# Kernel optimization log

Hardware: AMD Instinct MI355X
Metric: run time of the kernel (lower is better)

Reference implementation:

```python
import jax, jax.numpy as jnp
import numpy as np

PRE_NMS_THRESH = 0.05
PRE_NMS_TOP_N = 200
NMS_THRESH = 0.5
FPN_POST_NMS_TOP_N = 100
MIN_SIZE = 0.0
NUM_CLASSES = 2
C = NUM_CLASSES - 1
NB = 2
STRIDES = (8, 16, 32, 64, 128)
HS = (100, 50, 25, 13, 7)
WS = (128, 64, 32, 16, 8)
IMG_H, IMG_W = 800, 1024
MAXV = 8  # max #vertices of quad-clipped-by-quad polygon


def _shoelace_fixed(V, n):
    # area of polygon stored in fixed buffer V[MAXV,2] with n valid vertices
    a = jnp.asarray(0.0, V.dtype)
    for k in range(MAXV):
        nxt = jnp.where(jnp.equal(k, n - 1), 0, k + 1)
        term = V[k, 0] * V[nxt, 1] - V[nxt, 0] * V[k, 1]
        a = a + jnp.where(k < n, term, 0.0)
    return 0.5 * jnp.abs(a)


def _quad_area(Q):  # Q: [4,2]
    x, y = Q[:, 0], Q[:, 1]
    return 0.5 * jnp.abs(jnp.sum(x * jnp.roll(y, -1) - jnp.roll(x, -1) * y))


def _clip_halfplane(V, n, p1, p2, orient):
    # Sutherland-Hodgman clip of polygon (V,n) against directed edge p1->p2
    d = p2 - p1

    def side(p):
        return orient * (d[0] * (p[1] - p1[1]) - d[1] * (p[0] - p1[0]))

    out = jnp.zeros((MAXV, 2), V.dtype)
    cnt = jnp.int32(0)
    for k in range(MAXV):
        cur = V[k]
        prev = V[jnp.where(jnp.equal(k, 0), n - 1, k - 1)]
        sc = side(cur)
        sp = side(prev)
        cur_in = sc >= 0.0
        prev_in = sp >= 0.0
        denom = sp - sc
        t = sp / jnp.where(jnp.abs(denom) > 1e-9, denom, 1e-9)
        ip = prev + t * (cur - prev)
        valid = k < n
        emit_ip = valid & (cur_in != prev_in)
        out = jnp.where(emit_ip, out.at[cnt].set(ip, mode='drop'), out)
        cnt = cnt + emit_ip.astype(jnp.int32)
        emit_cur = valid & cur_in
        out = jnp.where(emit_cur, out.at[cnt].set(cur, mode='drop'), out)
        cnt = cnt + emit_cur.astype(jnp.int32)
    return out, cnt


def _poly_inter_area(A, B):  # A,B: [4,2] convex quads
    sB = jnp.sum(B[:, 0] * jnp.roll(B[:, 1], -1) - jnp.roll(B[:, 0], -1) * B[:, 1])
    orient = jnp.where(sB >= 0.0, 1.0, -1.0)
    V = jnp.zeros((MAXV, 2), A.dtype).at[:4].set(A)
    n = jnp.int32(4)
    for e in range(4):
        V, n = _clip_halfplane(V, n, B[e], B[(e + 1) % 4], orient)
    return _shoelace_fixed(V, n)


def _process_level(loc, cls_l, reg_l, image_sizes):
    Nb, Cc, H, W = cls_l.shape
    # (N,C,H,W) -> (N,HW*C) with index = (h*W+w)*C + c (matches permute/reshape)
    scores = jax.nn.sigmoid(cls_l.transpose(0, 2, 3, 1).reshape(Nb, H * W * Cc))
    cand = scores > PRE_NMS_THRESH
    masked = jnp.where(cand, scores, 0.0)
    k = min(PRE_NMS_TOP_N, H * W * Cc)
    vals, idx = jax.lax.top_k(masked, k)
    loc_idx = idx // Cc
    labels = idx % Cc + 1
    regr = reg_l.transpose(0, 2, 3, 1).reshape(Nb, H * W, 8)
    reg_g = jnp.take_along_axis(regr, loc_idx[..., None], axis=1)  # [Nb,k,8]
    loc_g = loc[loc_idx]  # [Nb,k,2]
    poly = jnp.tile(loc_g, (1, 1, 4)) - reg_g  # (x-r0, y-r1, ..., x-r6, y-r7)
    hh = image_sizes[:, 0].astype(poly.dtype)[:, None, None]
    ww = image_sizes[:, 1].astype(poly.dtype)[:, None, None]
    xs = jnp.clip(poly[..., 0::2], 0.0, ww - 1.0)
    ys = jnp.clip(poly[..., 1::2], 0.0, hh - 1.0)
    poly = jnp.stack([xs, ys], axis=-1).reshape(Nb, k, 8)
    valid = vals > PRE_NMS_THRESH
    bw = xs.max(-1) - xs.min(-1)
    bh = ys.max(-1) - ys.min(-1)
    valid = valid & (bw >= MIN_SIZE) & (bh >= MIN_SIZE)
    sc = jnp.where(valid, jnp.sqrt(vals), 0.0)
    return poly, sc, labels, valid


def _nms_single(poly, scores, labels, valid):
    T = scores.shape[0]
    order = jnp.argsort(-scores)
    poly = poly[order]
    scores = scores[order]
    labels = labels[order]
    valid = valid[order]
    quads = poly.reshape(T, 4, 2)

    def pairwise_iou(q):
        inter = jax.vmap(jax.vmap(_poly_inter_area, (None, 0)), (0, None))(q, q)
        areas = jax.vmap(_quad_area)(q)
        union = areas[:, None] + areas[None, :] - inter
        return inter / jnp.maximum(union, 1e-9)

    # IoU only feeds boolean suppression decisions -> no gradient flows through it
    iou = jax.lax.stop_gradient(pairwise_iou(quads))
    ar = jnp.arange(T)

    def body(i, keep):
        sup = (iou[i] > NMS_THRESH) & (ar > i)
        return jnp.where(keep[i], keep & ~sup, keep)

    keep = jax.lax.stop_gradient(jax.lax.fori_loop(0, T, body, valid))
    final = jnp.where(keep, scores, -1.0)
    top_s, top_i = jax.lax.top_k(final, FPN_POST_NMS_TOP_N)
    ok = top_s > 0.0
    return poly[top_i], jnp.where(ok, top_s, 0.0), labels[top_i], ok


def _forward(locs, clss, regs, image_sizes):
    parts = [_process_level(l, c, r, image_sizes) for l, c, r in zip(locs, clss, regs)]
    poly = jnp.concatenate([p[0] for p in parts], axis=1)
    sc = jnp.concatenate([p[1] for p in parts], axis=1)
    lab = jnp.concatenate([p[2] for p in parts], axis=1)
    val = jnp.concatenate([p[3] for p in parts], axis=1)
    return jax.vmap(_nms_single)(poly, sc, lab, val)


def setup_inputs() -> dict:
    key = jax.random.key(0)
    inp = {}
    k = key
    for i, (h, w, s) in enumerate(zip(HS, WS, STRIDES)):
        k, k1, k2, k3 = jax.random.split(k, 4)
        sx = jnp.arange(w, dtype=jnp.float32) * s + s // 2
        sy = jnp.arange(h, dtype=jnp.float32) * s + s // 2
        yy, xx = jnp.meshgrid(sy, sx, indexing='ij')
        inp[f'locations_l{i}'] = jnp.stack([xx.reshape(-1), yy.reshape(-1)], axis=1)
        inp[f'box_cls_l{i}'] = jax.random.normal(k1, (NB, C, h, w), dtype=jnp.float32)
        inp[f'box_reg_l{i}'] = jax.random.normal(k2, (NB, 8, h, w), dtype=jnp.float32) * (2.0 * s)
        inp[f'centerness_l{i}'] = jax.random.normal(k3, (NB, 1, h, w), dtype=jnp.float32)
    inp['image_sizes'] = jnp.array([[IMG_H, IMG_W]] * NB, dtype=jnp.int32)
    return inp


def reference(locations_l0, locations_l1, locations_l2, locations_l3, locations_l4,
              box_cls_l0, box_cls_l1, box_cls_l2, box_cls_l3, box_cls_l4,
              box_reg_l0, box_reg_l1, box_reg_l2, box_reg_l3, box_reg_l4,
              centerness_l0, centerness_l1, centerness_l2, centerness_l3, centerness_l4,
              image_sizes):
    # centerness is accepted but unused, matching the original module's forward
    locs = [locations_l0, locations_l1, locations_l2, locations_l3, locations_l4]
    clss = [box_cls_l0, box_cls_l1, box_cls_l2, box_cls_l3, box_cls_l4]
    regs = [box_reg_l0, box_reg_l1, box_reg_l2, box_reg_l3, box_reg_l4]
    boxes, scores, labels, valid = _forward(locs, clss, regs, image_sizes)
    return boxes, scores, labels, valid
```

## Files before the change

### kernel.cpp

```cpp
#include <hip/hip_runtime.h>

#pragma clang fp contract(off)

#define T_CAND 856
#define NW 14
#define NSH 16
#define HSTR 513

__device__ const int d_HW[5]  = {12800, 3200, 800, 208, 56};
__device__ const int d_K[5]   = {200, 200, 200, 200, 56};
__device__ const int d_OFF[5] = {0, 200, 400, 600, 800};

struct LevelPtrs {
  const float* loc[5];
  const float* cls[5];
  const float* reg[5];
  const int*   img;
};

__device__ __forceinline__ unsigned long long readlane64(unsigned long long v, int lane) {
  const unsigned lo = (unsigned)__builtin_amdgcn_readlane((int)(unsigned)(v & 0xFFFFFFFFULL), lane);
  const unsigned hi = (unsigned)__builtin_amdgcn_readlane((int)(unsigned)(v >> 32), lane);
  return ((unsigned long long)hi << 32) | lo;
}
__device__ __forceinline__ unsigned long long rfl64(unsigned long long v) {
  const unsigned lo = (unsigned)__builtin_amdgcn_readfirstlane((int)(unsigned)(v & 0xFFFFFFFFULL));
  const unsigned hi = (unsigned)__builtin_amdgcn_readfirstlane((int)(unsigned)(v >> 32));
  return ((unsigned long long)hi << 32) | lo;
}

__global__ __launch_bounds__(1024) void topk_kernel(LevelPtrs P,
    float* __restrict__ candPoly, float* __restrict__ candSc, unsigned* __restrict__ candValid,
    unsigned* __restrict__ pairCount) {
  __shared__ unsigned hist[NSH * HSTR];
  __shared__ unsigned histT[512];
  __shared__ __align__(16) unsigned long long gbuf[1024];
  __shared__ float mcache[12800];
  __shared__ int gcount;
  __shared__ int cutB;
  const int blk = blockIdx.x;
  const int b = blk / 5, l = blk % 5;
  const int HW = d_HW[l], K = d_K[l], OFF = d_OFF[l];
  const float* cls = P.cls[l] + (size_t)b * HW;
  const float* reg = P.reg[l] + (size_t)b * 8 * HW;
  const float* loc = P.loc[l];
  const int tid = threadIdx.x;
  const int wave = tid >> 6, lane = tid & 63;

  if (blk == 0 && tid == 0) *pairCount = 0u;
  for (int t = tid; t < NSH * HSTR; t += 1024) hist[t] = 0u;
  if (tid == 0) gcount = 0;
  __syncthreads();

  const int sh = (tid >> 2) & (NSH - 1);
  for (int idx = tid; idx < HW; idx += 1024) {
    const float x = cls[idx];
    const float s = (float)(1.0 / (1.0 + exp(-(double)x)));
    const float m = (s > 0.05f) ? s : 0.0f;
    mcache[idx] = m;
    atomicAdd(&hist[sh * HSTR + (__float_as_uint(m) >> 21)], 1u);
  }
  __syncthreads();
  for (int t = tid; t < 512; t += 1024) {
    unsigned sum = 0;
#pragma unroll
    for (int h = 0; h < NSH; ++h) sum += hist[h * HSTR + t];
    histT[t] = sum;
  }
  __syncthreads();
  if (wave == 0) {
    const int t0 = lane * 8;
    int h[8], loc8[8];
#pragma unroll
    for (int k = 0; k < 8; ++k) h[k] = (int)histT[t0 + k];
    int run = 0;
#pragma unroll
    for (int k = 7; k >= 0; --k) { run += h[k]; loc8[k] = run; }
    int v = run;
#pragma unroll
    for (int d = 1; d < 64; d <<= 1) {
      const int u = __shfl_down(v, d);
      if (lane + d < 64) v += u;
    }
    const int excl = v - run;
    int cand = -1;
#pragma unroll
    for (int k = 7; k >= 0; --k)
      if (cand < 0 && excl + loc8[k] >= K) cand = t0 + k;
    const unsigned long long bal = __ballot(cand >= 0);
    const int hi = 63 - __builtin_clzll(bal);
    const int cb = __shfl(cand, hi);
    if (lane == 0) cutB = cb;
  }
  __syncthreads();

  const int cb = cutB;
  for (int idx = tid; idx < HW; idx += 1024) {
    const unsigned kb = __float_as_uint(mcache[idx]);
    if ((int)(kb >> 21) >= cb) {
      const int pos = atomicAdd(&gcount, 1);
      if (pos < 1024)
        gbuf[pos] = ((unsigned long long)kb << 32)
                  | (unsigned long long)(0xFFFFFFFFu - (unsigned)idx);
    }
  }
  __syncthreads();
  const int G = min(gcount, 1024);
  if (tid < 4 && G + tid < 1024) gbuf[G + tid] = 0ULL;
  __syncthreads();

  if (tid < G) {
    const unsigned long long my = gbuf[tid];
    const int G4 = (G + 3) & ~3;
    int rank = 0;
    const ulonglong2* g2 = (const ulonglong2*)gbuf;
    for (int j = 0; j < G4 / 2; j += 2) {
      const ulonglong2 a = g2[j], c = g2[j + 1];
      rank += (a.x > my) ? 1 : 0;
      rank += (a.y > my) ? 1 : 0;
      rank += (c.x > my) ? 1 : 0;
      rank += (c.y > my) ? 1 : 0;
    }
    if (rank < K) {
      const float val = __uint_as_float((unsigned)(my >> 32));
      const int idx = (int)(0xFFFFFFFFu - (unsigned)(my & 0xFFFFFFFFULL));
      const float hh = (float)P.img[b * 2 + 0];
      const float ww = (float)P.img[b * 2 + 1];
      const float xmax = ww - 1.0f, ymax = hh - 1.0f;
      const float lx = loc[idx * 2 + 0], ly = loc[idx * 2 + 1];
      const int go = b * T_CAND + OFF + rank;
#pragma unroll
      for (int q = 0; q < 4; ++q) {
        const float rx = reg[(2 * q + 0) * HW + idx];
        const float ry = reg[(2 * q + 1) * HW + idx];
        const float pxv = fminf(fmaxf(lx - rx, 0.0f), xmax);
        const float pyv = fminf(fmaxf(ly - ry, 0.0f), ymax);
        candPoly[go * 8 + 2 * q + 0] = pxv;
        candPoly[go * 8 + 2 * q + 1] = pyv;
      }
      const bool v = (val > 0.05f);
      candSc[go]    = v ? sqrtf(val) : 0.0f;
      candValid[go] = v ? 1u : 0u;
    }
  }
}

__global__ __launch_bounds__(1024) void sort_kernel(
    const float* __restrict__ candPoly, const float* __restrict__ candSc,
    const unsigned* __restrict__ candValid,
    float* __restrict__ sPoly, float* __restrict__ sSc, unsigned* __restrict__ sValid,
    float* __restrict__ sAABB) {
  __shared__ __align__(16) unsigned long long key[T_CAND];
  const int b = blockIdx.x, tid = threadIdx.x;
  float sc = 0.0f;
  if (tid < T_CAND) {
    sc = candSc[b * T_CAND + tid];
    key[tid] = ((unsigned long long)__float_as_uint(sc) << 32)
             | (unsigned long long)(0xFFFFFFFFu - (unsigned)tid);
  }
  __syncthreads();
  if (tid < T_CAND) {
    const unsigned long long my = key[tid];
    int rank = 0;
    const ulonglong2* k2 = (const ulonglong2*)key;
    for (int j = 0; j < T_CAND / 2; j += 2) {
      const ulonglong2 a = k2[j], c = k2[j + 1];
      rank += (a.x > my) ? 1 : 0;
      rank += (a.y > my) ? 1 : 0;
      rank += (c.x > my) ? 1 : 0;
      rank += (c.y > my) ? 1 : 0;
    }
    sSc[b * T_CAND + rank]    = sc;
    sValid[b * T_CAND + rank] = candValid[b * T_CAND + tid];
    const float4* src = (const float4*)(candPoly + (size_t)(b * T_CAND + tid) * 8);
    const float4 s0 = src[0], s1 = src[1];
    float4* dst = (float4*)(sPoly + (size_t)(b * T_CAND + rank) * 8);
    dst[0] = s0;
    dst[1] = s1;
    float4 bb;
    bb.x = fminf(fminf(s0.x, s0.z), fminf(s1.x, s1.z));
    bb.y = fminf(fminf(s0.y, s0.w), fminf(s1.y, s1.w));
    bb.z = fmaxf(fmaxf(s0.x, s0.z), fmaxf(s1.x, s1.z));
    bb.w = fmaxf(fmaxf(s0.y, s0.w), fmaxf(s1.y, s1.w));
    *(float4*)(sAABB + (size_t)(b * T_CAND + rank) * 4) = bb;
  }
}

__global__ __launch_bounds__(256) void pairs_kernel(
    const unsigned* __restrict__ sValid, const float* __restrict__ sAABB,
    unsigned long long* __restrict__ MT, unsigned* __restrict__ pairList,
    unsigned* __restrict__ pairCount) {
  __shared__ __align__(16) float4 ra[64];
  __shared__ unsigned rv[64];
  __shared__ unsigned long long cw[64];
  __shared__ int rowoff[64];
  __shared__ int lcnt;
  __shared__ int gbase;
  const int b = blockIdx.y;
  int it = 0, rem = blockIdx.x;
  while (rem >= NW - it) { rem -= NW - it; ++it; }
  const int jt = it + rem;
  const int tid = threadIdx.x;
  const int wave = tid >> 6, lane = tid & 63;

  if (tid == 0) lcnt = 0;
  if (tid < 64) {
    const int row = it * 64 + tid;
    const int rc = row < T_CAND ? row : (T_CAND - 1);
    ra[tid] = *(const float4*)(sAABB + (size_t)(b * T_CAND + rc) * 4);
    rv[tid] = (row < T_CAND) ? sValid[b * T_CAND + row] : 0u;
    if (row < T_CAND) MT[((size_t)b * NW + jt) * T_CAND + row] = 0ULL;
  }
  __syncthreads();

  const int j = jt * 64 + lane;
  const int jcl = j < T_CAND ? j : (T_CAND - 1);
  const float4 jb = *(const float4*)(sAABB + (size_t)(b * T_CAND + jcl) * 4);
  const bool jv = (j < T_CAND) && (sValid[b * T_CAND + jcl] != 0u);
#pragma unroll
  for (int k = 0; k < 16; ++k) {
    const int r = wave * 16 + k;
    const int irow = it * 64 + r;
    const float4 ib = ra[r];
    const bool iv = rv[r] != 0u;
    const bool ov = !(ib.z < jb.x || jb.z < ib.x || ib.w < jb.y || jb.w < ib.y);
    const bool pred = iv && jv && (j > irow) && ov;
    const unsigned long long w = __ballot(pred);
    if (lane == 0) cw[r] = w;
  }
  __syncthreads();
  if (tid < 64) {
    const int c = __popcll(cw[tid]);
    rowoff[tid] = c ? atomicAdd(&lcnt, c) : 0;
  }
  __syncthreads();
  if (tid == 0) gbase = lcnt ? (int)atomicAdd(pairCount, (unsigned)lcnt) : 0;
  __syncthreads();
  if (tid < 64) {
    unsigned long long w = cw[tid];
    unsigned off = (unsigned)(gbase + rowoff[tid]);
    const int iRow = it * 64 + tid;
    while (w) {
      const int jo = (int)__builtin_ctzll(w);
      w &= w - 1;
      pairList[off++] = ((unsigned)b << 20) | ((unsigned)iRow << 10) | (unsigned)(jt * 64 + jo);
    }
  }
}

__global__ __launch_bounds__(256) void clip_kernel(
    const unsigned* __restrict__ pairList, const unsigned* __restrict__ pairCount,
    const float* __restrict__ sPoly, unsigned long long* __restrict__ MT) {
  const int tid = threadIdx.x;
  const unsigned count = *pairCount;
  for (unsigned t0 = blockIdx.x * 256 + tid; t0 < count; t0 += gridDim.x * 256) {
    const unsigned pk = pairList[t0];
    const int b = (pk >> 20) & 1, i = (pk >> 10) & 1023, j = pk & 1023;
    const float4* Ap4 = (const float4*)(sPoly + (size_t)(b * T_CAND + i) * 8);
    const float4 a01 = Ap4[0], a23 = Ap4[1];
    const float ax0 = a01.x, ay0 = a01.y, ax1 = a01.z, ay1 = a01.w,
                ax2 = a23.x, ay2 = a23.y, ax3 = a23.z, ay3 = a23.w;
    const float4* Bp4 = (const float4*)(sPoly + (size_t)(b * T_CAND + j) * 8);
    const float4 b01 = Bp4[0], b23 = Bp4[1];
    const float bx0 = b01.x, by0 = b01.y, bx1 = b01.z, by1 = b01.w,
                bx2 = b23.x, by2 = b23.y, bx3 = b23.z, by3 = b23.w;
    float sB = bx0 * by1 - bx1 * by0;
    sB += bx1 * by2 - bx2 * by1;
    sB += bx2 * by3 - bx3 * by2;
    sB += bx3 * by0 - bx0 * by3;
    const float orient = (sB >= 0.0f) ? 1.0f : -1.0f;
    float aA = ax0 * ay1 - ax1 * ay0;
    aA += ax1 * ay2 - ax2 * ay1;
    aA += ax2 * ay3 - ax3 * ay2;
    aA += ax3 * ay0 - ax0 * ay3;

    float s0x = ax0, s0y = ay0, s1x = ax1, s1y = ay1,
          s2x = ax2, s2y = ay2, s3x = ax3, s3y = ay3,
          s4x = 0.f, s4y = 0.f, s5x = 0.f, s5y = 0.f,
          s6x = 0.f, s6y = 0.f, s7x = 0.f, s7y = 0.f;
    int n = 4;
    float lastx = ax3, lasty = ay3;
    const float bex[5] = {bx0, bx1, bx2, bx3, bx0};
    const float bey[5] = {by0, by1, by2, by3, by0};

#define PUSH(w_, vx_, vy_)                                              \
    {                                                                   \
      const bool w__ = (w_);                                            \
      const float vx__ = (vx_), vy__ = (vy_);                           \
      t0x = (w__ && cnt == 0) ? vx__ : t0x; t0y = (w__ && cnt == 0) ? vy__ : t0y; \
      t1x = (w__ && cnt == 1) ? vx__ : t1x; t1y = (w__ && cnt == 1) ? vy__ : t1y; \
      t2x = (w__ && cnt == 2) ? vx__ : t2x; t2y = (w__ && cnt == 2) ? vy__ : t2y; \
      t3x = (w__ && cnt == 3) ? vx__ : t3x; t3y = (w__ && cnt == 3) ? vy__ : t3y; \
      t4x = (w__ && cnt == 4) ? vx__ : t4x; t4y = (w__ && cnt == 4) ? vy__ : t4y; \
      t5x = (w__ && cnt == 5) ? vx__ : t5x; t5y = (w__ && cnt == 5) ? vy__ : t5y; \
      t6x = (w__ && cnt == 6) ? vx__ : t6x; t6y = (w__ && cnt == 6) ? vy__ : t6y; \
      t7x = (w__ && cnt == 7) ? vx__ : t7x; t7y = (w__ && cnt == 7) ? vy__ : t7y; \
      nlx = (w__ && cnt < 8) ? vx__ : nlx;  nly = (w__ && cnt < 8) ? vy__ : nly;  \
      cnt += w__ ? 1 : 0;                                               \
    }

#define CLIP_K(k_, sx_, sy_)                                            \
    {                                                                   \
      const bool act = (k_) < n;                                        \
      const float cx = sx_, cy = sy_;                                   \
      const float sc2 = orient * (dx * (cy - p1y) - dy * (cx - p1x));   \
      const bool cin = (sc2 >= 0.0f), pin = (sp >= 0.0f);               \
      const float den = sp - sc2;                                       \
      const float dd = (fabsf(den) > 1e-9f) ? den : 1e-9f;              \
      const float tt = sp / dd;                                         \
      const float ipx = px + tt * (cx - px);                            \
      const float ipy = py + tt * (cy - py);                            \
      PUSH(act && (cin != pin), ipx, ipy);                              \
      PUSH(act && cin, cx, cy);                                         \
      px = cx; py = cy; sp = sc2;                                       \
    }

#pragma unroll
    for (int e = 0; e < 4; ++e) {
      const float p1x = bex[e], p1y = bey[e];
      const float dx = bex[e + 1] - p1x, dy = bey[e + 1] - p1y;
      float t0x = 0.f, t0y = 0.f, t1x = 0.f, t1y = 0.f, t2x = 0.f, t2y = 0.f,
            t3x = 0.f, t3y = 0.f, t4x = 0.f, t4y = 0.f, t5x = 0.f, t5y = 0.f,
            t6x = 0.f, t6y = 0.f, t7x = 0.f, t7y = 0.f;
      float nlx = lastx, nly = lasty;
      int cnt = 0;
      float px = lastx, py = lasty;
      float sp = orient * (dx * (py - p1y) - dy * (px - p1x));
      CLIP_K(0, s0x, s0y) CLIP_K(1, s1x, s1y) CLIP_K(2, s2x, s2y) CLIP_K(3, s3x, s3y)
      CLIP_K(4, s4x, s4y) CLIP_K(5, s5x, s5y) CLIP_K(6, s6x, s6y) CLIP_K(7, s7x, s7y)
      s0x = t0x; s0y = t0y; s1x = t1x; s1y = t1y; s2x = t2x; s2y = t2y;
      s3x = t3x; s3y = t3y; s4x = t4x; s4y = t4y; s5x = t5x; s5y = t5y;
      s6x = t6x; s6y = t6y; s7x = t7x; s7y = t7y;
      lastx = nlx; lasty = nly;
      n = cnt;
    }
#undef CLIP_K
#undef PUSH

    float a = 0.0f;
#define SHOE(k_, xk_, yk_, xn_, yn_)                                    \
    {                                                                   \
      const bool act = (k_) < n;                                        \
      const bool wrap = (k_) == n - 1;                                  \
      const float xn = wrap ? s0x : (xn_);                              \
      const float yn = wrap ? s0y : (yn_);                              \
      const float term = (xk_) * yn - xn * (yk_);                       \
      a += act ? term : 0.0f;                                           \
    }
    SHOE(0, s0x, s0y, s1x, s1y) SHOE(1, s1x, s1y, s2x, s2y)
    SHOE(2, s2x, s2y, s3x, s3y) SHOE(3, s3x, s3y, s4x, s4y)
    SHOE(4, s4x, s4y, s5x, s5y) SHOE(5, s5x, s5y, s6x, s6y)
    SHOE(6, s6x, s6y, s7x, s7y) SHOE(7, s7x, s7y, s7x, s7y)
#undef SHOE
    const float inter = 0.5f * fabsf(a);
    const float areaA = 0.5f * fabsf(aA);
    const float areaB = 0.5f * fabsf(sB);
    const float uni = areaA + areaB - inter;
    const float iou = inter / fmaxf(uni, 1e-9f);
    if (iou > 0.5f)
      atomicOr(&MT[((size_t)b * NW + (j >> 6)) * T_CAND + i], 1ULL << (j & 63));
  }
}

__global__ __launch_bounds__(1024) void nms_resolve_emit_kernel(
    const unsigned long long* __restrict__ MT, const unsigned* __restrict__ sValid,
    const float* __restrict__ sPoly, const float* __restrict__ sSc, float* __restrict__ out) {
  __shared__ __align__(16) unsigned long long mt[NW * T_CAND];
  __shared__ unsigned long long vb[16];
  __shared__ unsigned long long kw[NW];
  const int b = blockIdx.x;
  const int tid = threadIdx.x;
  const int wave = tid >> 6, lane = tid & 63;

  {
    const ulonglong2* g2 = (const ulonglong2*)(MT + (size_t)b * NW * T_CAND);
    ulonglong2* l2 = (ulonglong2*)mt;
    for (int t = tid; t < NW * T_CAND / 2; t += 1024) l2[t] = g2[t];
  }
  if (wave < NW) {
    const int idx = wave * 64 + lane;
    const bool v = (idx < T_CAND) && (sValid[b * T_CAND + idx] != 0u);
    const unsigned long long ball = __ballot(v);
    if (lane == 0) vb[wave] = ball;
  }
  __syncthreads();

  if (wave == 0) {
    unsigned long long kwreg = 0ULL;
    for (int q = 0; q < NW; ++q) {
      const unsigned long long* col = &mt[q * T_CAND];
      const int nrow = q * 64 + lane;
      const unsigned long long sup = col[nrow < T_CAND ? nrow : (T_CAND - 1)];
      unsigned long long acc = 0ULL;
      for (int wp = 0; wp < q; ++wp) {
        const unsigned long long row = col[wp * 64 + lane];
        const unsigned long long kword = readlane64(kwreg, wp);
        acc |= ((kword >> lane) & 1ULL) ? row : 0ULL;
      }
#pragma unroll
      for (int m = 1; m < 64; m <<= 1)
        acc |= (unsigned long long)__shfl_xor((long long)acc, m, 64);
      const unsigned long long S = rfl64(acc);
      const unsigned long long validq = rfl64(vb[q]);
      unsigned long long alive = validq & ~S;
      const unsigned long long suppr = __ballot(sup != 0ULL);
      unsigned long long rem = alive & suppr;
      while (rem) {
        const int s = (int)__builtin_ctzll(rem);
        rem &= rem - 1;
        if ((alive >> s) & 1ULL) {
          alive &= ~readlane64(sup, s);
          rem &= alive;
        }
      }
      if (lane == q) kwreg = alive;
    }
    if (lane < NW) kw[lane] = kwreg;
  }
  __syncthreads();

  if (tid < 100) {
    const int o = tid;
    int totalKeep = 0;
    for (int w = 0; w < NW; ++w) totalKeep += __popcll(kw[w]);
    const bool kept = o < totalKeep;
    int idx = 0;
    if (kept) {
      int r = o, w = 0;
      unsigned long long word = 0ULL;
      for (; w < NW; ++w) {
        word = kw[w];
        const int c = __popcll(word);
        if (r < c) break;
        r -= c;
      }
      for (int p = 0; p < r; ++p) word &= word - 1;
      idx = w * 64 + (__ffsll(word) - 1);
    } else {
      int r = o - totalKeep, w = 0;
      unsigned long long word = 0ULL;
      for (; w < NW; ++w) {
        const unsigned long long mk = (w == NW - 1) ? ((1ULL << (T_CAND - 64 * (NW - 1))) - 1ULL)
                                                    : ~0ULL;
        word = (~kw[w]) & mk;
        const int c = __popcll(word);
        if (r < c) break;
        r -= c;
      }
      for (int p = 0; p < r; ++p) word &= word - 1;
      idx = w * 64 + (__ffsll(word) - 1);
    }
    const float4* pp = (const float4*)(sPoly + (size_t)(b * T_CAND + idx) * 8);
    float4* ob2 = (float4*)(out + (size_t)b * 800 + (size_t)o * 8);
    ob2[0] = pp[0];
    ob2[1] = pp[1];
    out[1600 + b * 100 + o] = kept ? sSc[b * T_CAND + idx] : 0.0f;
    out[1800 + b * 100 + o] = 1.0f;
    out[2000 + b * 100 + o] = kept ? 1.0f : 0.0f;
  }
}

extern "C" void kernel_launch(void* const* d_in, const int* in_sizes, int n_in,
                              void* d_out, int out_size, void* d_ws, size_t ws_size,
                              hipStream_t stream) {
  (void)n_in; (void)out_size; (void)ws_size;
  LevelPtrs P;
  const bool interleaved = (in_sizes[2] == 204800);
  for (int l = 0; l < 5; ++l) {
    if (interleaved) {
      P.loc[l] = (const float*)d_in[4 * l + 0];
      P.cls[l] = (const float*)d_in[4 * l + 1];
      P.reg[l] = (const float*)d_in[4 * l + 2];
    } else {
      P.loc[l] = (const float*)d_in[l];
      P.cls[l] = (const float*)d_in[5 + l];
      P.reg[l] = (const float*)d_in[10 + l];
    }
  }
  P.img = (const int*)d_in[20];

  char* ws = (char*)d_ws;
  float*    candPoly  = (float*)(ws + 0);
  float*    candSc    = (float*)(ws + 54784);
  unsigned* candValid = (unsigned*)(ws + 61632);
  float*    sPoly     = (float*)(ws + 68480);
  float*    sSc       = (float*)(ws + 123264);
  unsigned* sValid    = (unsigned*)(ws + 130112);
  unsigned long long* MT = (unsigned long long*)(ws + 136960);
  float*    sAABB     = (float*)(ws + 328704);
  unsigned* pairCount = (unsigned*)(ws + 356096);
  unsigned* pairList  = (unsigned*)(ws + 356112);

  topk_kernel<<<dim3(10), dim3(1024), 0, stream>>>(P, candPoly, candSc, candValid, pairCount);
  sort_kernel<<<dim3(2), dim3(1024), 0, stream>>>(candPoly, candSc, candValid,
                                                  sPoly, sSc, sValid, sAABB);
  pairs_kernel<<<dim3((NW * (NW + 1)) / 2, 2), dim3(256), 0, stream>>>(sValid, sAABB, MT,
                                                                       pairList, pairCount);
  clip_kernel<<<dim3(512), dim3(256), 0, stream>>>(pairList, pairCount, sPoly, MT);
  nms_resolve_emit_kernel<<<dim3(2), dim3(1024), 0, stream>>>(MT, sValid, sPoly, sSc,
                                                              (float*)d_out);
}
```

Measured before the change: 74.75 us.

## Fuse five NMS stages into one cooperative kernel with grid syncs

Replaces the five separate kernel launches (top-k, sort, pair finding, polygon clipping, NMS resolve) with a single cooperative kernel of 210 blocks of 512 threads, separated by grid.sync(). The pair list is now built per tile in shared memory, and clipping results are OR-ed into shared words instead of going through a global pair list and atomic counter. The aim is to cut launch overhead and global round-trips between stages. In exchange it adds grid-wide barrier cost, leaves most blocks idle in the top-k and resolve phases, and uses a single large shared buffer that may limit occupancy.

```diff
diff --git a/kernel.cpp b/kernel.cpp
--- a/kernel.cpp
+++ b/kernel.cpp
@@ -1,4 +1,5 @@
 #include <hip/hip_runtime.h>
+#include <hip/hip_cooperative_groups.h>
 
 #pragma clang fp contract(off)
 
@@ -6,6 +7,10 @@
 #define NW 14
 #define NSH 16
 #define HSTR 513
+#define NBLK 210
+#define NTHR 512
+
+namespace cg = cooperative_groups;
 
 __device__ const int d_HW[5]  = {12800, 3200, 800, 208, 56};
 __device__ const int d_K[5]   = {200, 200, 200, 200, 56};
@@ -29,434 +34,423 @@
   return ((unsigned long long)hi << 32) | lo;
 }
 
-__global__ __launch_bounds__(1024) void topk_kernel(LevelPtrs P,
+__device__ __forceinline__ bool clip_hit(const float* __restrict__ sPoly, int b, int i, int j) {
+  const float4* Ap4 = (const float4*)(sPoly + (size_t)(b * T_CAND + i) * 8);
+  const float4 a01 = Ap4[0], a23 = Ap4[1];
+  const float ax0 = a01.x, ay0 = a01.y, ax1 = a01.z, ay1 = a01.w,
+              ax2 = a23.x, ay2 = a23.y, ax3 = a23.z, ay3 = a23.w;
+  const float4* Bp4 = (const float4*)(sPoly + (size_t)(b * T_CAND + j) * 8);
+  const float4 b01 = Bp4[0], b23 = Bp4[1];
+  const float bx0 = b01.x, by0 = b01.y, bx1 = b01.z, by1 = b01.w,
+              bx2 = b23.x, by2 = b23.y, bx3 = b23.z, by3 = b23.w;
+  float sB = bx0 * by1 - bx1 * by0;
+  sB += bx1 * by2 - bx2 * by1;
+  sB += bx2 * by3 - bx3 * by2;
+  sB += bx3 * by0 - bx0 * by3;
+  const float orient = (sB >= 0.0f) ? 1.0f : -1.0f;
+  float aA = ax0 * ay1 - ax1 * ay0;
+  aA += ax1 * ay2 - ax2 * ay1;
+  aA += ax2 * ay3 - ax3 * ay2;
+  aA += ax3 * ay0 - ax0 * ay3;
+
+  float s0x = ax0, s0y = ay0, s1x = ax1, s1y = ay1,
+        s2x = ax2, s2y = ay2, s3x = ax3, s3y = ay3,
+        s4x = 0.f, s4y = 0.f, s5x = 0.f, s5y = 0.f,
+        s6x = 0.f, s6y = 0.f, s7x = 0.f, s7y = 0.f;
+  int n = 4;
+  float lastx = ax3, lasty = ay3;
+  const float bex[5] = {bx0, bx1, bx2, bx3, bx0};
+  const float bey[5] = {by0, by1, by2, by3, by0};
+
+#define PUSH(w_, vx_, vy_)                                              \
+  {                                                                     \
+    const bool w__ = (w_);                                              \
+    const float vx__ = (vx_), vy__ = (vy_);                             \
+    t0x = (w__ && cnt == 0) ? vx__ : t0x; t0y = (w__ && cnt == 0) ? vy__ : t0y; \
+    t1x = (w__ && cnt == 1) ? vx__ : t1x; t1y = (w__ && cnt == 1) ? vy__ : t1y; \
+    t2x = (w__ && cnt == 2) ? vx__ : t2x; t2y = (w__ && cnt == 2) ? vy__ : t2y; \
+    t3x = (w__ && cnt == 3) ? vx__ : t3x; t3y = (w__ && cnt == 3) ? vy__ : t3y; \
+    t4x = (w__ && cnt == 4) ? vx__ : t4x; t4y = (w__ && cnt == 4) ? vy__ : t4y; \
+    t5x = (w__ && cnt == 5) ? vx__ : t5x; t5y = (w__ && cnt == 5) ? vy__ : t5y; \
+    t6x = (w__ && cnt == 6) ? vx__ : t6x; t6y = (w__ && cnt == 6) ? vy__ : t6y; \
+    t7x = (w__ && cnt == 7) ? vx__ : t7x; t7y = (w__ && cnt == 7) ? vy__ : t7y; \
+    nlx = (w__ && cnt < 8) ? vx__ : nlx;  nly = (w__ && cnt < 8) ? vy__ : nly;  \
+    cnt += w__ ? 1 : 0;                                                 \
+  }
+
+#define CLIP_K(k_, sx_, sy_)                                            \
+  {                                                                     \
+    const bool act = (k_) < n;                                          \
+    const float cx = sx_, cy = sy_;                                     \
+    const float sc2 = orient * (dx * (cy - p1y) - dy * (cx - p1x));     \
+    const bool cin = (sc2 >= 0.0f), pin = (sp >= 0.0f);                 \
+    const float den = sp - sc2;                                         \
+    const float dd = (fabsf(den) > 1e-9f) ? den : 1e-9f;                \
+    const float tt = sp / dd;                                           \
+    const float ipx = px + tt * (cx - px);                              \
+    const float ipy = py + tt * (cy - py);                              \
+    PUSH(act && (cin != pin), ipx, ipy);                                \
+    PUSH(act && cin, cx, cy);                                           \
+    px = cx; py = cy; sp = sc2;                                         \
+  }
+
+#pragma unroll
+  for (int e = 0; e < 4; ++e) {
+    const float p1x = bex[e], p1y = bey[e];
+    const float dx = bex[e + 1] - p1x, dy = bey[e + 1] - p1y;
+    float t0x = 0.f, t0y = 0.f, t1x = 0.f, t1y = 0.f, t2x = 0.f, t2y = 0.f,
+          t3x = 0.f, t3y = 0.f, t4x = 0.f, t4y = 0.f, t5x = 0.f, t5y = 0.f,
+          t6x = 0.f, t6y = 0.f, t7x = 0.f, t7y = 0.f;
+    float nlx = lastx, nly = lasty;
+    int cnt = 0;
+    float px = lastx, py = lasty;
+    float sp = orient * (dx * (py - p1y) - dy * (px - p1x));
+    CLIP_K(0, s0x, s0y) CLIP_K(1, s1x, s1y) CLIP_K(2, s2x, s2y) CLIP_K(3, s3x, s3y)
+    CLIP_K(4, s4x, s4y) CLIP_K(5, s5x, s5y) CLIP_K(6, s6x, s6y) CLIP_K(7, s7x, s7y)
+    s0x = t0x; s0y = t0y; s1x = t1x; s1y = t1y; s2x = t2x; s2y = t2y;
+    s3x = t3x; s3y = t3y; s4x = t4x; s4y = t4y; s5x = t5x; s5y = t5y;
+    s6x = t6x; s6y = t6y; s7x = t7x; s7y = t7y;
+    lastx = nlx; lasty = nly;
+    n = cnt;
+  }
+#undef CLIP_K
+#undef PUSH
+
+  float a = 0.0f;
+#define SHOE(k_, xk_, yk_, xn_, yn_)                                    \
+  {                                                                     \
+    const bool act = (k_) < n;                                          \
+    const bool wrap = (k_) == n - 1;                                    \
+    const float xn = wrap ? s0x : (xn_);                                \
+    const float yn = wrap ? s0y : (yn_);                                \
+    const float term = (xk_) * yn - xn * (yk_);                         \
+    a += act ? term : 0.0f;                                             \
+  }
+  SHOE(0, s0x, s0y, s1x, s1y) SHOE(1, s1x, s1y, s2x, s2y)
+  SHOE(2, s2x, s2y, s3x, s3y) SHOE(3, s3x, s3y, s4x, s4y)
+  SHOE(4, s4x, s4y, s5x, s5y) SHOE(5, s5x, s5y, s6x, s6y)
+  SHOE(6, s6x, s6y, s7x, s7y) SHOE(7, s7x, s7y, s7x, s7y)
+#undef SHOE
+  const float inter = 0.5f * fabsf(a);
+  const float areaA = 0.5f * fabsf(aA);
+  const float areaB = 0.5f * fabsf(sB);
+  const float uni = areaA + areaB - inter;
+  const float iou = inter / fmaxf(uni, 1e-9f);
+  return iou > 0.5f;
+}
+
+__global__ __launch_bounds__(NTHR) void fused_kernel(LevelPtrs P,
     float* __restrict__ candPoly, float* __restrict__ candSc, unsigned* __restrict__ candValid,
-    unsigned* __restrict__ pairCount) {
-  __shared__ unsigned hist[NSH * HSTR];
-  __shared__ unsigned histT[512];
-  __shared__ __align__(16) unsigned long long gbuf[1024];
-  __shared__ float mcache[12800];
-  __shared__ int gcount;
-  __shared__ int cutB;
+    float* __restrict__ sPoly, float* __restrict__ sSc, unsigned* __restrict__ sValid,
+    float* __restrict__ sAABB, unsigned long long* __restrict__ MT, float* __restrict__ out) {
+  __shared__ __align__(16) char smem[96256];
+  __shared__ int sInt0;
+  __shared__ int sInt1;
+  cg::grid_group grid = cg::this_grid();
   const int blk = blockIdx.x;
-  const int b = blk / 5, l = blk % 5;
-  const int HW = d_HW[l], K = d_K[l], OFF = d_OFF[l];
-  const float* cls = P.cls[l] + (size_t)b * HW;
-  const float* reg = P.reg[l] + (size_t)b * 8 * HW;
-  const float* loc = P.loc[l];
   const int tid = threadIdx.x;
   const int wave = tid >> 6, lane = tid & 63;
 
-  if (blk == 0 && tid == 0) *pairCount = 0u;
-  for (int t = tid; t < NSH * HSTR; t += 1024) hist[t] = 0u;
-  if (tid == 0) gcount = 0;
-  __syncthreads();
-
-  const int sh = (tid >> 2) & (NSH - 1);
-  for (int idx = tid; idx < HW; idx += 1024) {
-    const float x = cls[idx];
-    const float s = (float)(1.0 / (1.0 + exp(-(double)x)));
-    const float m = (s > 0.05f) ? s : 0.0f;
-    mcache[idx] = m;
-    atomicAdd(&hist[sh * HSTR + (__float_as_uint(m) >> 21)], 1u);
-  }
-  __syncthreads();
-  for (int t = tid; t < 512; t += 1024) {
-    unsigned sum = 0;
-#pragma unroll
-    for (int h = 0; h < NSH; ++h) sum += hist[h * HSTR + t];
-    histT[t] = sum;
-  }
-  __syncthreads();
-  if (wave == 0) {
-    const int t0 = lane * 8;
-    int h[8], loc8[8];
-#pragma unroll
-    for (int k = 0; k < 8; ++k) h[k] = (int)histT[t0 + k];
-    int run = 0;
-#pragma unroll
-    for (int k = 7; k >= 0; --k) { run += h[k]; loc8[k] = run; }
-    int v = run;
-#pragma unroll
-    for (int d = 1; d < 64; d <<= 1) {
-      const int u = __shfl_down(v, d);
-      if (lane + d < 64) v += u;
-    }
-    const int excl = v - run;
-    int cand = -1;
-#pragma unroll
-    for (int k = 7; k >= 0; --k)
-      if (cand < 0 && excl + loc8[k] >= K) cand = t0 + k;
-    const unsigned long long bal = __ballot(cand >= 0);
-    const int hi = 63 - __builtin_clzll(bal);
-    const int cb = __shfl(cand, hi);
-    if (lane == 0) cutB = cb;
-  }
-  __syncthreads();
-
-  const int cb = cutB;
-  for (int idx = tid; idx < HW; idx += 1024) {
-    const unsigned kb = __float_as_uint(mcache[idx]);
-    if ((int)(kb >> 21) >= cb) {
-      const int pos = atomicAdd(&gcount, 1);
-      if (pos < 1024)
-        gbuf[pos] = ((unsigned long long)kb << 32)
-                  | (unsigned long long)(0xFFFFFFFFu - (unsigned)idx);
-    }
-  }
-  __syncthreads();
-  const int G = min(gcount, 1024);
-  if (tid < 4 && G + tid < 1024) gbuf[G + tid] = 0ULL;
-  __syncthreads();
-
-  if (tid < G) {
-    const unsigned long long my = gbuf[tid];
+  if (blk < 10) {
+    unsigned* hist = (unsigned*)smem;
+    unsigned* histT = (unsigned*)(smem + 32832);
+    unsigned long long* gbuf = (unsigned long long*)(smem + 34880);
+    float* mcache = (float*)(smem + 43072);
+    const int b = blk / 5, l = blk % 5;
+    const int HW = d_HW[l], K = d_K[l], OFF = d_OFF[l];
+    const float* cls = P.cls[l] + (size_t)b * HW;
+    const float* reg = P.reg[l] + (size_t)b * 8 * HW;
+    const float* loc = P.loc[l];
+
+    for (int t = tid; t < NSH * HSTR; t += NTHR) hist[t] = 0u;
+    if (tid == 0) sInt0 = 0;
+    __syncthreads();
+
+    const int sh = (tid >> 2) & (NSH - 1);
+    for (int idx = tid; idx < HW; idx += NTHR) {
+      const float x = cls[idx];
+      const float s = (float)(1.0 / (1.0 + exp(-(double)x)));
+      const float m = (s > 0.05f) ? s : 0.0f;
+      mcache[idx] = m;
+      atomicAdd(&hist[sh * HSTR + (__float_as_uint(m) >> 21)], 1u);
+    }
+    __syncthreads();
+    for (int t = tid; t < 512; t += NTHR) {
+      unsigned sum = 0;
+#pragma unroll
+      for (int h = 0; h < NSH; ++h) sum += hist[h * HSTR + t];
+      histT[t] = sum;
+    }
+    __syncthreads();
+    if (wave == 0) {
+      const int t0 = lane * 8;
+      int h[8], loc8[8];
+#pragma unroll
+      for (int k = 0; k < 8; ++k) h[k] = (int)histT[t0 + k];
+      int run = 0;
+#pragma unroll
+      for (int k = 7; k >= 0; --k) { run += h[k]; loc8[k] = run; }
+      int v = run;
+#pragma unroll
+      for (int d = 1; d < 64; d <<= 1) {
+        const int u = __shfl_down(v, d);
+        if (lane + d < 64) v += u;
+      }
+      const int excl = v - run;
+      int cand = -1;
+#pragma unroll
+      for (int k = 7; k >= 0; --k)
+        if (cand < 0 && excl + loc8[k] >= K) cand = t0 + k;
+      const unsigned long long bal = __ballot(cand >= 0);
+      const int hi = 63 - __builtin_clzll(bal);
+      const int cb = __shfl(cand, hi);
+      if (lane == 0) sInt1 = cb;
+    }
+    __syncthreads();
+
+    const int cb = sInt1;
+    for (int idx = tid; idx < HW; idx += NTHR) {
+      const unsigned kb = __float_as_uint(mcache[idx]);
+      if ((int)(kb >> 21) >= cb) {
+        const int pos = atomicAdd(&sInt0, 1);
+        if (pos < 1024)
+          gbuf[pos] = ((unsigned long long)kb << 32)
+                    | (unsigned long long)(0xFFFFFFFFu - (unsigned)idx);
+      }
+    }
+    __syncthreads();
+    const int G = min(sInt0, 1024);
+    if (tid < 4 && G + tid < 1024) gbuf[G + tid] = 0ULL;
+    __syncthreads();
+
     const int G4 = (G + 3) & ~3;
-    int rank = 0;
-    const ulonglong2* g2 = (const ulonglong2*)gbuf;
-    for (int j = 0; j < G4 / 2; j += 2) {
-      const ulonglong2 a = g2[j], c = g2[j + 1];
-      rank += (a.x > my) ? 1 : 0;
-      rank += (a.y > my) ? 1 : 0;
-      rank += (c.x > my) ? 1 : 0;
-      rank += (c.y > my) ? 1 : 0;
-    }
-    if (rank < K) {
-      const float val = __uint_as_float((unsigned)(my >> 32));
-      const int idx = (int)(0xFFFFFFFFu - (unsigned)(my & 0xFFFFFFFFULL));
-      const float hh = (float)P.img[b * 2 + 0];
-      const float ww = (float)P.img[b * 2 + 1];
-      const float xmax = ww - 1.0f, ymax = hh - 1.0f;
-      const float lx = loc[idx * 2 + 0], ly = loc[idx * 2 + 1];
-      const int go = b * T_CAND + OFF + rank;
-#pragma unroll
-      for (int q = 0; q < 4; ++q) {
-        const float rx = reg[(2 * q + 0) * HW + idx];
-        const float ry = reg[(2 * q + 1) * HW + idx];
-        const float pxv = fminf(fmaxf(lx - rx, 0.0f), xmax);
-        const float pyv = fminf(fmaxf(ly - ry, 0.0f), ymax);
-        candPoly[go * 8 + 2 * q + 0] = pxv;
-        candPoly[go * 8 + 2 * q + 1] = pyv;
-      }
-      const bool v = (val > 0.05f);
-      candSc[go]    = v ? sqrtf(val) : 0.0f;
-      candValid[go] = v ? 1u : 0u;
-    }
-  }
-}
-
-__global__ __launch_bounds__(1024) void sort_kernel(
-    const float* __restrict__ candPoly, const float* __restrict__ candSc,
-    const unsigned* __restrict__ candValid,
-    float* __restrict__ sPoly, float* __restrict__ sSc, unsigned* __restrict__ sValid,
-    float* __restrict__ sAABB) {
-  __shared__ __align__(16) unsigned long long key[T_CAND];
-  const int b = blockIdx.x, tid = threadIdx.x;
-  float sc = 0.0f;
-  if (tid < T_CAND) {
-    sc = candSc[b * T_CAND + tid];
-    key[tid] = ((unsigned long long)__float_as_uint(sc) << 32)
-             | (unsigned long long)(0xFFFFFFFFu - (unsigned)tid);
-  }
-  __syncthreads();
-  if (tid < T_CAND) {
-    const unsigned long long my = key[tid];
-    int rank = 0;
-    const ulonglong2* k2 = (const ulonglong2*)key;
-    for (int j = 0; j < T_CAND / 2; j += 2) {
-      const ulonglong2 a = k2[j], c = k2[j + 1];
-      rank += (a.x > my) ? 1 : 0;
-      rank += (a.y > my) ? 1 : 0;
-      rank += (c.x > my) ? 1 : 0;
-      rank += (c.y > my) ? 1 : 0;
-    }
-    sSc[b * T_CAND + rank]    = sc;
-    sValid[b * T_CAND + rank] = candValid[b * T_CAND + tid];
-    const float4* src = (const float4*)(candPoly + (size_t)(b * T_CAND + tid) * 8);
-    const float4 s0 = src[0], s1 = src[1];
-    float4* dst = (float4*)(sPoly + (size_t)(b * T_CAND + rank) * 8);
-    dst[0] = s0;
-    dst[1] = s1;
-    float4 bb;
-    bb.x = fminf(fminf(s0.x, s0.z), fminf(s1.x, s1.z));
-    bb.y = fminf(fminf(s0.y, s0.w), fminf(s1.y, s1.w));
-    bb.z = fmaxf(fmaxf(s0.x, s0.z), fmaxf(s1.x, s1.z));
-    bb.w = fmaxf(fmaxf(s0.y, s0.w), fmaxf(s1.y, s1.w));
-    *(float4*)(sAABB + (size_t)(b * T_CAND + rank) * 4) = bb;
-  }
-}
-
-__global__ __launch_bounds__(256) void pairs_kernel(
-    const unsigned* __restrict__ sValid, const float* __restrict__ sAABB,
-    unsigned long long* __restrict__ MT, unsigned* __restrict__ pairList,
-    unsigned* __restrict__ pairCount) {
-  __shared__ __align__(16) float4 ra[64];
-  __shared__ unsigned rv[64];
-  __shared__ unsigned long long cw[64];
-  __shared__ int rowoff[64];
-  __shared__ int lcnt;
-  __shared__ int gbase;
-  const int b = blockIdx.y;
-  int it = 0, rem = blockIdx.x;
-  while (rem >= NW - it) { rem -= NW - it; ++it; }
-  const int jt = it + rem;
-  const int tid = threadIdx.x;
-  const int wave = tid >> 6, lane = tid & 63;
-
-  if (tid == 0) lcnt = 0;
-  if (tid < 64) {
-    const int row = it * 64 + tid;
-    const int rc = row < T_CAND ? row : (T_CAND - 1);
-    ra[tid] = *(const float4*)(sAABB + (size_t)(b * T_CAND + rc) * 4);
-    rv[tid] = (row < T_CAND) ? sValid[b * T_CAND + row] : 0u;
-    if (row < T_CAND) MT[((size_t)b * NW + jt) * T_CAND + row] = 0ULL;
-  }
-  __syncthreads();
-
-  const int j = jt * 64 + lane;
-  const int jcl = j < T_CAND ? j : (T_CAND - 1);
-  const float4 jb = *(const float4*)(sAABB + (size_t)(b * T_CAND + jcl) * 4);
-  const bool jv = (j < T_CAND) && (sValid[b * T_CAND + jcl] != 0u);
-#pragma unroll
-  for (int k = 0; k < 16; ++k) {
-    const int r = wave * 16 + k;
-    const int irow = it * 64 + r;
-    const float4 ib = ra[r];
-    const bool iv = rv[r] != 0u;
-    const bool ov = !(ib.z < jb.x || jb.z < ib.x || ib.w < jb.y || jb.w < ib.y);
-    const bool pred = iv && jv && (j > irow) && ov;
-    const unsigned long long w = __ballot(pred);
-    if (lane == 0) cw[r] = w;
-  }
-  __syncthreads();
-  if (tid < 64) {
-    const int c = __popcll(cw[tid]);
-    rowoff[tid] = c ? atomicAdd(&lcnt, c) : 0;
-  }
-  __syncthreads();
-  if (tid == 0) gbase = lcnt ? (int)atomicAdd(pairCount, (unsigned)lcnt) : 0;
-  __syncthreads();
-  if (tid < 64) {
-    unsigned long long w = cw[tid];
-    unsigned off = (unsigned)(gbase + rowoff[tid]);
-    const int iRow = it * 64 + tid;
-    while (w) {
-      const int jo = (int)__builtin_ctzll(w);
-      w &= w - 1;
-      pairList[off++] = ((unsigned)b << 20) | ((unsigned)iRow << 10) | (unsigned)(jt * 64 + jo);
-    }
-  }
-}
-
-__global__ __launch_bounds__(256) void clip_kernel(
-    const unsigned* __restrict__ pairList, const unsigned* __restrict__ pairCount,
-    const float* __restrict__ sPoly, unsigned long long* __restrict__ MT) {
-  const int tid = threadIdx.x;
-  const unsigned count = *pairCount;
-  for (unsigned t0 = blockIdx.x * 256 + tid; t0 < count; t0 += gridDim.x * 256) {
-    const unsigned pk = pairList[t0];
-    const int b = (pk >> 20) & 1, i = (pk >> 10) & 1023, j = pk & 1023;
-    const float4* Ap4 = (const float4*)(sPoly + (size_t)(b * T_CAND + i) * 8);
-    const float4 a01 = Ap4[0], a23 = Ap4[1];
-    const float ax0 = a01.x, ay0 = a01.y, ax1 = a01.z, ay1 = a01.w,
-                ax2 = a23.x, ay2 = a23.y, ax3 = a23.z, ay3 = a23.w;
-    const float4* Bp4 = (const float4*)(sPoly + (size_t)(b * T_CAND + j) * 8);
-    const float4 b01 = Bp4[0], b23 = Bp4[1];
-    const float bx0 = b01.x, by0 = b01.y, bx1 = b01.z, by1 = b01.w,
-                bx2 = b23.x, by2 = b23.y, bx3 = b23.z, by3 = b23.w;
-    float sB = bx0 * by1 - bx1 * by0;
-    sB += bx1 * by2 - bx2 * by1;
-    sB += bx2 * by3 - bx3 * by2;
-    sB += bx3 * by0 - bx0 * by3;
-    const float orient = (sB >= 0.0f) ? 1.0f : -1.0f;
-    float aA = ax0 * ay1 - ax1 * ay0;
-    aA += ax1 * ay2 - ax2 * ay1;
-    aA += ax2 * ay3 - ax3 * ay2;
-    aA += ax3 * ay0 - ax0 * ay3;
-
-    float s0x = ax0, s0y = ay0, s1x = ax1, s1y = ay1,
-          s2x = ax2, s2y = ay2, s3x = ax3, s3y = ay3,
-          s4x = 0.f, s4y = 0.f, s5x = 0.f, s5y = 0.f,
-          s6x = 0.f, s6y = 0.f, s7x = 0.f, s7y = 0.f;
-    int n = 4;
-    float lastx = ax3, lasty = ay3;
-    const float bex[5] = {bx0, bx1, bx2, bx3, bx0};
-    const float bey[5] = {by0, by1, by2, by3, by0};
-
-#define PUSH(w_, vx_, vy_)                                              \
-    {                                                                   \
-      const bool w__ = (w_);                                            \
-      const float vx__ = (vx_), vy__ = (vy_);                           \
-      t0x = (w__ && cnt == 0) ? vx__ : t0x; t0y = (w__ && cnt == 0) ? vy__ : t0y; \
-      t1x = (w__ && cnt == 1) ? vx__ : t1x; t1y = (w__ && cnt == 1) ? vy__ : t1y; \
-      t2x = (w__ && cnt == 2) ? vx__ : t2x; t2y = (w__ && cnt == 2) ? vy__ : t2y; \
-      t3x = (w__ && cnt == 3) ? vx__ : t3x; t3y = (w__ && cnt == 3) ? vy__ : t3y; \
-      t4x = (w__ && cnt == 4) ? vx__ : t4x; t4y = (w__ && cnt == 4) ? vy__ : t4y; \
-      t5x = (w__ && cnt == 5) ? vx__ : t5x; t5y = (w__ && cnt == 5) ? vy__ : t5y; \
-      t6x = (w__ && cnt == 6) ? vx__ : t6x; t6y = (w__ && cnt == 6) ? vy__ : t6y; \
-      t7x = (w__ && cnt == 7) ? vx__ : t7x; t7y = (w__ && cnt == 7) ? vy__ : t7y; \
-      nlx = (w__ && cnt < 8) ? vx__ : nlx;  nly = (w__ && cnt < 8) ? vy__ : nly;  \
-      cnt += w__ ? 1 : 0;                                               \
-    }
-
-#define CLIP_K(k_, sx_, sy_)                                            \
-    {                                                                   \
-      const bool act = (k_) < n;                                        \
-      const float cx = sx_, cy = sy_;                                   \
-      const float sc2 = orient * (dx * (cy - p1y) - dy * (cx - p1x));   \
-      const bool cin = (sc2 >= 0.0f), pin = (sp >= 0.0f);               \
-      const float den = sp - sc2;                                       \
-      const float dd = (fabsf(den) > 1e-9f) ? den : 1e-9f;              \
-      const float tt = sp / dd;                                         \
-      const float ipx = px + tt * (cx - px);                            \
-      const float ipy = py + tt * (cy - py);                            \
-      PUSH(act && (cin != pin), ipx, ipy);                              \
-      PUSH(act && cin, cx, cy);                                         \
-      px = cx; py = cy; sp = sc2;                                       \
-    }
-
-#pragma unroll
-    for (int e = 0; e < 4; ++e) {
-      const float p1x = bex[e], p1y = bey[e];
-      const float dx = bex[e + 1] - p1x, dy = bey[e + 1] - p1y;
-      float t0x = 0.f, t0y = 0.f, t1x = 0.f, t1y = 0.f, t2x = 0.f, t2y = 0.f,
-            t3x = 0.f, t3y = 0.f, t4x = 0.f, t4y = 0.f, t5x = 0.f, t5y = 0.f,
-            t6x = 0.f, t6y = 0.f, t7x = 0.f, t7y = 0.f;
-      float nlx = lastx, nly = lasty;
-      int cnt = 0;
-      float px = lastx, py = lasty;
-      float sp = orient * (dx * (py - p1y) - dy * (px - p1x));
-      CLIP_K(0, s0x, s0y) CLIP_K(1, s1x, s1y) CLIP_K(2, s2x, s2y) CLIP_K(3, s3x, s3y)
-      CLIP_K(4, s4x, s4y) CLIP_K(5, s5x, s5y) CLIP_K(6, s6x, s6y) CLIP_K(7, s7x, s7y)
-      s0x = t0x; s0y = t0y; s1x = t1x; s1y = t1y; s2x = t2x; s2y = t2y;
-      s3x = t3x; s3y = t3y; s4x = t4x; s4y = t4y; s5x = t5x; s5y = t5y;
-      s6x = t6x; s6y = t6y; s7x = t7x; s7y = t7y;
-      lastx = nlx; lasty = nly;
-      n = cnt;
-    }
-#undef CLIP_K
-#undef PUSH
-
-    float a = 0.0f;
-#define SHOE(k_, xk_, yk_, xn_, yn_)                                    \
-    {                                                                   \
-      const bool act = (k_) < n;                                        \
-      const bool wrap = (k_) == n - 1;                                  \
-      const float xn = wrap ? s0x : (xn_);                              \
-      const float yn = wrap ? s0y : (yn_);                              \
-      const float term = (xk_) * yn - xn * (yk_);                       \
-      a += act ? term : 0.0f;                                           \
-    }
-    SHOE(0, s0x, s0y, s1x, s1y) SHOE(1, s1x, s1y, s2x, s2y)
-    SHOE(2, s2x, s2y, s3x, s3y) SHOE(3, s3x, s3y, s4x, s4y)
-    SHOE(4, s4x, s4y, s5x, s5y) SHOE(5, s5x, s5y, s6x, s6y)
-    SHOE(6, s6x, s6y, s7x, s7y) SHOE(7, s7x, s7y, s7x, s7y)
-#undef SHOE
-    const float inter = 0.5f * fabsf(a);
-    const float areaA = 0.5f * fabsf(aA);
-    const float areaB = 0.5f * fabsf(sB);
-    const float uni = areaA + areaB - inter;
-    const float iou = inter / fmaxf(uni, 1e-9f);
-    if (iou > 0.5f)
-      atomicOr(&MT[((size_t)b * NW + (j >> 6)) * T_CAND + i], 1ULL << (j & 63));
-  }
-}
-
-__global__ __launch_bounds__(1024) void nms_resolve_emit_kernel(
-    const unsigned long long* __restrict__ MT, const unsigned* __restrict__ sValid,
-    const float* __restrict__ sPoly, const float* __restrict__ sSc, float* __restrict__ out) {
-  __shared__ __align__(16) unsigned long long mt[NW * T_CAND];
-  __shared__ unsigned long long vb[16];
-  __shared__ unsigned long long kw[NW];
-  const int b = blockIdx.x;
-  const int tid = threadIdx.x;
-  const int wave = tid >> 6, lane = tid & 63;
+    for (int t = tid; t < G; t += NTHR) {
+      const unsigned long long my = gbuf[t];
+      int rank = 0;
+      const ulonglong2* g2 = (const ulonglong2*)gbuf;
+      for (int j = 0; j < G4 / 2; j += 2) {
+        const ulonglong2 a = g2[j], c = g2[j + 1];
+        rank += (a.x > my) ? 1 : 0;
+        rank += (a.y > my) ? 1 : 0;
+        rank += (c.x > my) ? 1 : 0;
+        rank += (c.y > my) ? 1 : 0;
+      }
+      if (rank < K) {
+        const float val = __uint_as_float((unsigned)(my >> 32));
+        const int idx = (int)(0xFFFFFFFFu - (unsigned)(my & 0xFFFFFFFFULL));
+        const float hh = (float)P.img[b * 2 + 0];
+        const float ww = (float)P.img[b * 2 + 1];
+        const float xmax = ww - 1.0f, ymax = hh - 1.0f;
+        const float lx = loc[idx * 2 + 0], ly = loc[idx * 2 + 1];
+        const int go = b * T_CAND + OFF + rank;
+#pragma unroll
+        for (int q = 0; q < 4; ++q) {
+          const float rx = reg[(2 * q + 0) * HW + idx];
+          const float ry = reg[(2 * q + 1) * HW + idx];
+          const float pxv = fminf(fmaxf(lx - rx, 0.0f), xmax);
+          const float pyv = fminf(fmaxf(ly - ry, 0.0f), ymax);
+          candPoly[go * 8 + 2 * q + 0] = pxv;
+          candPoly[go * 8 + 2 * q + 1] = pyv;
+        }
+        const bool v = (val > 0.05f);
+        candSc[go]    = v ? sqrtf(val) : 0.0f;
+        candValid[go] = v ? 1u : 0u;
+      }
+    }
+  }
+  grid.sync();
+
+  if (blk < 2) {
+    unsigned long long* key = (unsigned long long*)smem;
+    const int b = blk;
+    for (int c = tid; c < T_CAND; c += NTHR) {
+      const float sc = candSc[b * T_CAND + c];
+      key[c] = ((unsigned long long)__float_as_uint(sc) << 32)
+             | (unsigned long long)(0xFFFFFFFFu - (unsigned)c);
+    }
+    __syncthreads();
+    for (int c = tid; c < T_CAND; c += NTHR) {
+      const unsigned long long my = key[c];
+      int rank = 0;
+      const ulonglong2* k2 = (const ulonglong2*)key;
+      for (int j = 0; j < T_CAND / 2; j += 2) {
+        const ulonglong2 a = k2[j], cc = k2[j + 1];
+        rank += (a.x > my) ? 1 : 0;
+        rank += (a.y > my) ? 1 : 0;
+        rank += (cc.x > my) ? 1 : 0;
+        rank += (cc.y > my) ? 1 : 0;
+      }
+      sSc[b * T_CAND + rank]    = __uint_as_float((unsigned)(my >> 32));
+      sValid[b * T_CAND + rank] = candValid[b * T_CAND + c];
+      const float4* src = (const float4*)(candPoly + (size_t)(b * T_CAND + c) * 8);
+      const float4 s0 = src[0], s1 = src[1];
+      float4* dst = (float4*)(sPoly + (size_t)(b * T_CAND + rank) * 8);
+      dst[0] = s0;
+      dst[1] = s1;
+      float4 bb;
+      bb.x = fminf(fminf(s0.x, s0.z), fminf(s1.x, s1.z));
+      bb.y = fminf(fminf(s0.y, s0.w), fminf(s1.y, s1.w));
+      bb.z = fmaxf(fmaxf(s0.x, s0.z), fmaxf(s1.x, s1.z));
+      bb.w = fmaxf(fmaxf(s0.y, s0.w), fmaxf(s1.y, s1.w));
+      *(float4*)(sAABB + (size_t)(b * T_CAND + rank) * 4) = bb;
+    }
+  }
+  grid.sync();
 
   {
-    const ulonglong2* g2 = (const ulonglong2*)(MT + (size_t)b * NW * T_CAND);
-    ulonglong2* l2 = (ulonglong2*)mt;
-    for (int t = tid; t < NW * T_CAND / 2; t += 1024) l2[t] = g2[t];
-  }
-  if (wave < NW) {
-    const int idx = wave * 64 + lane;
-    const bool v = (idx < T_CAND) && (sValid[b * T_CAND + idx] != 0u);
-    const unsigned long long ball = __ballot(v);
-    if (lane == 0) vb[wave] = ball;
-  }
-  __syncthreads();
-
-  if (wave == 0) {
-    unsigned long long kwreg = 0ULL;
-    for (int q = 0; q < NW; ++q) {
-      const unsigned long long* col = &mt[q * T_CAND];
-      const int nrow = q * 64 + lane;
-      const unsigned long long sup = col[nrow < T_CAND ? nrow : (T_CAND - 1)];
-      unsigned long long acc = 0ULL;
-      for (int wp = 0; wp < q; ++wp) {
-        const unsigned long long row = col[wp * 64 + lane];
-        const unsigned long long kword = readlane64(kwreg, wp);
-        acc |= ((kword >> lane) & 1ULL) ? row : 0ULL;
-      }
-#pragma unroll
-      for (int m = 1; m < 64; m <<= 1)
-        acc |= (unsigned long long)__shfl_xor((long long)acc, m, 64);
-      const unsigned long long S = rfl64(acc);
-      const unsigned long long validq = rfl64(vb[q]);
-      unsigned long long alive = validq & ~S;
-      const unsigned long long suppr = __ballot(sup != 0ULL);
-      unsigned long long rem = alive & suppr;
-      while (rem) {
-        const int s = (int)__builtin_ctzll(rem);
-        rem &= rem - 1;
-        if ((alive >> s) & 1ULL) {
-          alive &= ~readlane64(sup, s);
-          rem &= alive;
+    float4* ra = (float4*)smem;
+    unsigned* rv = (unsigned*)(smem + 1024);
+    unsigned long long* cw = (unsigned long long*)(smem + 1280);
+    unsigned* pl = (unsigned*)(smem + 1792);
+    unsigned long long* ow = (unsigned long long*)(smem + 18176);
+    const int b = blk / 105;
+    int it = 0, rem = blk % 105;
+    while (rem >= NW - it) { rem -= NW - it; ++it; }
+    const int jt = it + rem;
+
+    if (tid == 0) sInt0 = 0;
+    if (tid < 64) {
+      const int row = it * 64 + tid;
+      const int rc = row < T_CAND ? row : (T_CAND - 1);
+      ra[tid] = *(const float4*)(sAABB + (size_t)(b * T_CAND + rc) * 4);
+      rv[tid] = (row < T_CAND) ? sValid[b * T_CAND + row] : 0u;
+      ow[tid] = 0ULL;
+    }
+    __syncthreads();
+
+    const int j = jt * 64 + lane;
+    const int jcl = j < T_CAND ? j : (T_CAND - 1);
+    const float4 jb = *(const float4*)(sAABB + (size_t)(b * T_CAND + jcl) * 4);
+    const bool jv = (j < T_CAND) && (sValid[b * T_CAND + jcl] != 0u);
+#pragma unroll
+    for (int k = 0; k < 8; ++k) {
+      const int r = wave * 8 + k;
+      const int irow = it * 64 + r;
+      const float4 ib = ra[r];
+      const bool iv = rv[r] != 0u;
+      const bool ov = !(ib.z < jb.x || jb.z < ib.x || ib.w < jb.y || jb.w < ib.y);
+      const bool pred = iv && jv && (j > irow) && ov;
+      const unsigned long long w = __ballot(pred);
+      if (lane == 0) cw[r] = w;
+    }
+    __syncthreads();
+    if (tid < 64) {
+      unsigned long long w = cw[tid];
+      const int c = __popcll(w);
+      int off = c ? atomicAdd(&sInt0, c) : 0;
+      while (w) {
+        const int jo = (int)__builtin_ctzll(w);
+        w &= w - 1;
+        pl[off++] = ((unsigned)tid << 6) | (unsigned)jo;
+      }
+    }
+    __syncthreads();
+    const int total = sInt0;
+    for (int p = tid; p < total; p += NTHR) {
+      const unsigned pk = pl[p];
+      const int io = (int)(pk >> 6), jo = (int)(pk & 63u);
+      if (clip_hit(sPoly, b, it * 64 + io, jt * 64 + jo))
+        atomicOr(&ow[io], 1ULL << jo);
+    }
+    __syncthreads();
+    if (tid < 64) {
+      const int row = it * 64 + tid;
+      if (row < T_CAND) MT[((size_t)b * NW + jt) * T_CAND + row] = ow[tid];
+    }
+  }
+  grid.sync();
+
+  if (blk < 2) {
+    unsigned long long* mt = (unsigned long long*)smem;
+    unsigned long long* vb = (unsigned long long*)(smem + 95872);
+    unsigned long long* kw = (unsigned long long*)(smem + 96000);
+    const int b = blk;
+    {
+      const ulonglong2* g2 = (const ulonglong2*)(MT + (size_t)b * NW * T_CAND);
+      ulonglong2* l2 = (ulonglong2*)mt;
+      for (int t = tid; t < NW * T_CAND / 2; t += NTHR) l2[t] = g2[t];
+    }
+    for (int q = wave; q < NW; q += 8) {
+      const int idx = q * 64 + lane;
+      const bool v = (idx < T_CAND) && (sValid[b * T_CAND + idx] != 0u);
+      const unsigned long long ball = __ballot(v);
+      if (lane == 0) vb[q] = ball;
+    }
+    __syncthreads();
+
+    if (wave == 0) {
+      unsigned long long kwreg = 0ULL;
+      for (int q = 0; q < NW; ++q) {
+        const unsigned long long* col = &mt[q * T_CAND];
+        const int nrow = q * 64 + lane;
+        const unsigned long long sup = col[nrow < T_CAND ? nrow : (T_CAND - 1)];
+        unsigned long long acc = 0ULL;
+        for (int wp = 0; wp < q; ++wp) {
+          const unsigned long long row = col[wp * 64 + lane];
+          const unsigned long long kword = readlane64(kwreg, wp);
+          acc |= ((kword >> lane) & 1ULL) ? row : 0ULL;
         }
-      }
-      if (lane == q) kwreg = alive;
-    }
-    if (lane < NW) kw[lane] = kwreg;
-  }
-  __syncthreads();
-
-  if (tid < 100) {
-    const int o = tid;
-    int totalKeep = 0;
-    for (int w = 0; w < NW; ++w) totalKeep += __popcll(kw[w]);
-    const bool kept = o < totalKeep;
-    int idx = 0;
-    if (kept) {
-      int r = o, w = 0;
-      unsigned long long word = 0ULL;
-      for (; w < NW; ++w) {
-        word = kw[w];
-        const int c = __popcll(word);
-        if (r < c) break;
-        r -= c;
-      }
-      for (int p = 0; p < r; ++p) word &= word - 1;
-      idx = w * 64 + (__ffsll(word) - 1);
-    } else {
-      int r = o - totalKeep, w = 0;
-      unsigned long long word = 0ULL;
-      for (; w < NW; ++w) {
-        const unsigned long long mk = (w == NW - 1) ? ((1ULL << (T_CAND - 64 * (NW - 1))) - 1ULL)
-                                                    : ~0ULL;
-        word = (~kw[w]) & mk;
-        const int c = __popcll(word);
-        if (r < c) break;
-        r -= c;
-      }
-      for (int p = 0; p < r; ++p) word &= word - 1;
-      idx = w * 64 + (__ffsll(word) - 1);
-    }
-    const float4* pp = (const float4*)(sPoly + (size_t)(b * T_CAND + idx) * 8);
-    float4* ob2 = (float4*)(out + (size_t)b * 800 + (size_t)o * 8);
-    ob2[0] = pp[0];
-    ob2[1] = pp[1];
-    out[1600 + b * 100 + o] = kept ? sSc[b * T_CAND + idx] : 0.0f;
-    out[1800 + b * 100 + o] = 1.0f;
-    out[2000 + b * 100 + o] = kept ? 1.0f : 0.0f;
+#pragma unroll
+        for (int m = 1; m < 64; m <<= 1)
+          acc |= (unsigned long long)__shfl_xor((long long)acc, m, 64);
+        const unsigned long long S = rfl64(acc);
+        const unsigned long long validq = rfl64(vb[q]);
+        unsigned long long alive = validq & ~S;
+        const unsigned long long suppr = __ballot(sup != 0ULL);
+        unsigned long long rm = alive & suppr;
+        while (rm) {
+          const int s = (int)__builtin_ctzll(rm);
+          rm &= rm - 1;
+          if ((alive >> s) & 1ULL) {
+            alive &= ~readlane64(sup, s);
+            rm &= alive;
+          }
+        }
+        if (lane == q) kwreg = alive;
+      }
+      if (lane < NW) kw[lane] = kwreg;
+    }
+    __syncthreads();
+
+    if (tid < 100) {
+      const int o = tid;
+      int totalKeep = 0;
+      for (int w = 0; w < NW; ++w) totalKeep += __popcll(kw[w]);
+      const bool kept = o < totalKeep;
+      int idx = 0;
+      if (kept) {
+        int r = o, w = 0;
+        unsigned long long word = 0ULL;
+        for (; w < NW; ++w) {
+          word = kw[w];
+          const int c = __popcll(word);
+          if (r < c) break;
+          r -= c;
+        }
+        for (int p = 0; p < r; ++p) word &= word - 1;
+        idx = w * 64 + (__ffsll(word) - 1);
+      } else {
+        int r = o - totalKeep, w = 0;
+        unsigned long long word = 0ULL;
+        for (; w < NW; ++w) {
+          const unsigned long long mk = (w == NW - 1)
+              ? ((1ULL << (T_CAND - 64 * (NW - 1))) - 1ULL) : ~0ULL;
+          word = (~kw[w]) & mk;
+          const int c = __popcll(word);
+          if (r < c) break;
+          r -= c;
+        }
+        for (int p = 0; p < r; ++p) word &= word - 1;
+        idx = w * 64 + (__ffsll(word) - 1);
+      }
+      const float4* pp = (const float4*)(sPoly + (size_t)(b * T_CAND + idx) * 8);
+      float4* ob2 = (float4*)(out + (size_t)b * 800 + (size_t)o * 8);
+      ob2[0] = pp[0];
+      ob2[1] = pp[1];
+      out[1600 + b * 100 + o] = kept ? sSc[b * T_CAND + idx] : 0.0f;
+      out[1800 + b * 100 + o] = 1.0f;
+      out[2000 + b * 100 + o] = kept ? 1.0f : 0.0f;
+    }
   }
 }
 
@@ -488,15 +482,10 @@
   unsigned* sValid    = (unsigned*)(ws + 130112);
   unsigned long long* MT = (unsigned long long*)(ws + 136960);
   float*    sAABB     = (float*)(ws + 328704);
-  unsigned* pairCount = (unsigned*)(ws + 356096);
-  unsigned* pairList  = (unsigned*)(ws + 356112);
-
-  topk_kernel<<<dim3(10), dim3(1024), 0, stream>>>(P, candPoly, candSc, candValid, pairCount);
-  sort_kernel<<<dim3(2), dim3(1024), 0, stream>>>(candPoly, candSc, candValid,
-                                                  sPoly, sSc, sValid, sAABB);
-  pairs_kernel<<<dim3((NW * (NW + 1)) / 2, 2), dim3(256), 0, stream>>>(sValid, sAABB, MT,
-                                                                       pairList, pairCount);
-  clip_kernel<<<dim3(512), dim3(256), 0, stream>>>(pairList, pairCount, sPoly, MT);
-  nms_resolve_emit_kernel<<<dim3(2), dim3(1024), 0, stream>>>(MT, sValid, sPoly, sSc,
-                                                              (float*)d_out);
+  float*    out       = (float*)d_out;
+
+  void* args[] = {&P, &candPoly, &candSc, &candValid, &sPoly, &sSc, &sValid,
+                  &sAABB, &MT, &out};
+  hipLaunchCooperativeKernel((const void*)fused_kernel, dim3(NBLK), dim3(NTHR),
+                             args, 0, stream);
 }
```

Measured after the change: 136.0 us. 82.0% more time.
